# Kernel tuning notes

Hardware: AMD Instinct MI355X
Metric: run time of the kernel (lower is better)

## Reference

```python
import jax, jax.numpy as jnp
import numpy as np

NUM_NODES = 100000
NUM_HYPEREDGES = 20000
NUM_INCIDENCE = 1600000  # E: total (node, hyperedge) incidence entries
IN_CH = 128
OUT_CH = 128
EPS = 1e-6


def setup_inputs() -> dict:
    key = jax.random.key(0)
    k_x, k_row, k_col, k_w, k_b = jax.random.split(key, 5)
    x = jax.random.normal(k_x, (NUM_NODES, IN_CH), dtype=jnp.float32)
    node_idx = jax.random.randint(k_row, (NUM_INCIDENCE,), 0, NUM_NODES, dtype=jnp.int64)
    edge_idx = jax.random.randint(k_col, (NUM_INCIDENCE,), 0, NUM_HYPEREDGES, dtype=jnp.int64)
    hyperedge_index = jnp.stack([node_idx, edge_idx], axis=0)
    theta_w = jax.random.normal(k_w, (OUT_CH, IN_CH), dtype=jnp.float32) / np.sqrt(IN_CH)
    theta_b = jax.random.normal(k_b, (OUT_CH,), dtype=jnp.float32) * 0.01
    hyperedge_weight = jnp.ones((NUM_HYPEREDGES,), dtype=jnp.float32)
    return {"x": x, "hyperedge_index": hyperedge_index, "theta_w": theta_w,
            "theta_b": theta_b, "hyperedge_weight": hyperedge_weight}


def reference(x, hyperedge_index, theta_w, theta_b, hyperedge_weight):
    node_idx = hyperedge_index[0]  # [E]
    edge_idx = hyperedge_index[1]  # [E]
    ones_e = jnp.ones(node_idx.shape[0], dtype=x.dtype)

    # degree normalizers: B = hyperedge degrees, D = node degrees
    b_inv = 1.0 / (jax.ops.segment_sum(ones_e, edge_idx, num_segments=NUM_HYPEREDGES) + EPS)
    d_inv = 1.0 / (jax.ops.segment_sum(ones_e, node_idx, num_segments=NUM_NODES) + EPS)

    # X' = x @ Theta^T + b
    x_t = x @ theta_w.T + theta_b  # [N, out]

    # H^T X': scatter node features into hyperedges
    edge_feat = jax.ops.segment_sum(x_t[node_idx], edge_idx, num_segments=NUM_HYPEREDGES)
    edge_feat = edge_feat * (b_inv * hyperedge_weight)[:, None]  # [M, out]

    # H (W B^-1 H^T X'): scatter hyperedge features back to nodes
    node_agg = jax.ops.segment_sum(edge_feat[edge_idx], node_idx, num_segments=NUM_NODES)
    return node_agg * d_inv[:, None]  # [N, out]
```

## Files before the change

### kernel.cpp

```cpp
#include <hip/hip_runtime.h>

#define N_NODES 100000
#define N_EDGES 20000
#define CH 128
#define EPS 1e-6f

#define GEMM_BLOCKS ((N_NODES + 63) / 64)
#define NXCD 8
#define EPG ((N_EDGES + NXCD - 1) / NXCD)
#define NPG ((N_NODES + NXCD - 1) / NXCD)

#define CAP_E 192
#define CAP_N 64

typedef __attribute__((ext_vector_type(8))) short bf16x8;
typedef __attribute__((ext_vector_type(4))) float f32x4;

__device__ __forceinline__ unsigned short f2bf(float f) {
    unsigned int u = __float_as_uint(f);
    return (unsigned short)((u + 0x7FFFu + ((u >> 16) & 1u)) >> 16);
}
__device__ __forceinline__ float bflo(unsigned int u) { return __uint_as_float(u << 16); }
__device__ __forceinline__ float bfhi(unsigned int u) { return __uint_as_float(u & 0xFFFF0000u); }

__global__ __launch_bounds__(256) void wcvt_kernel(
    const float* __restrict__ w, unsigned short* __restrict__ wbf) {
    int i = blockIdx.x * 256 + threadIdx.x;
    if (i < CH * CH) wbf[i] = f2bf(w[i]);
}

__global__ __launch_bounds__(256) void gemm_kernel(
    const float* __restrict__ x, const unsigned short* __restrict__ wbf,
    const float* __restrict__ bias, unsigned short* __restrict__ xt) {

    const int l = threadIdx.x & 63;
    const int wv = threadIdx.x >> 6;
    const int rbase = blockIdx.x * 64 + wv * 16;
    const int arow = rbase + (l & 15);
    const int kb = (l >> 4) * 8;
    const bool rok = (arow < N_NODES);

    bf16x8 afr[4];
#pragma unroll
    for (int ks = 0; ks < 4; ++ks) {
        if (rok) {
            const float* xp = x + (size_t)arow * CH + ks * 32 + kb;
            float4 v0 = *(const float4*)xp;
            float4 v1 = *(const float4*)(xp + 4);
            afr[ks][0] = (short)f2bf(v0.x); afr[ks][1] = (short)f2bf(v0.y);
            afr[ks][2] = (short)f2bf(v0.z); afr[ks][3] = (short)f2bf(v0.w);
            afr[ks][4] = (short)f2bf(v1.x); afr[ks][5] = (short)f2bf(v1.y);
            afr[ks][6] = (short)f2bf(v1.z); afr[ks][7] = (short)f2bf(v1.w);
        } else {
#pragma unroll
            for (int i = 0; i < 8; ++i) afr[ks][i] = 0;
        }
    }

    const int r0 = (l >> 4) * 4;
#pragma unroll
    for (int nt = 0; nt < 8; ++nt) {
        const int bcol = nt * 16 + (l & 15);
        float bv = bias[bcol];
        f32x4 acc;
        acc[0] = bv; acc[1] = bv; acc[2] = bv; acc[3] = bv;
#pragma unroll
        for (int ks = 0; ks < 4; ++ks) {
            bf16x8 bfr = *(const bf16x8*)(wbf + (size_t)bcol * CH + ks * 32 + kb);
            acc = __builtin_amdgcn_mfma_f32_16x16x32_bf16(afr[ks], bfr, acc, 0, 0, 0);
        }
#pragma unroll
        for (int r = 0; r < 4; ++r) {
            int grow = rbase + r0 + r;
            if (grow < N_NODES)
                xt[(size_t)grow * CH + bcol] = f2bf(acc[r]);
        }
    }
}

__global__ __launch_bounds__(256) void fill_kernel(
    const int* __restrict__ node_idx, const int* __restrict__ edge_idx, int E,
    int* __restrict__ ecur, int* __restrict__ ncur,
    int* __restrict__ elist, int* __restrict__ nlist) {
    const int g = blockIdx.x & (NXCD - 1);
    const int wid = blockIdx.x >> 3;
    const int nblk = gridDim.x >> 3;
    const int elo = g * EPG, ehi = min(elo + EPG, N_EDGES);
    const int nlo = g * NPG, nhi = min(nlo + NPG, N_NODES);

    int i = wid * blockDim.x + threadIdx.x;
    const int stride = nblk * blockDim.x;
    for (; i < E; i += stride) {
        int e = edge_idx[i];
        int n = node_idx[i];
        if (e >= elo && e < ehi) {
            int p = atomicAdd(&ecur[e], 1);
            if (p < CAP_E) elist[(size_t)e * CAP_E + p] = n;
        }
        if (n >= nlo && n < nhi) {
            int q = atomicAdd(&ncur[n], 1);
            if (q < CAP_N) nlist[(size_t)n * CAP_N + q] = e;
        }
    }
}

__global__ __launch_bounds__(256) void edge_agg_kernel(
    const unsigned short* __restrict__ xt, const int* __restrict__ elist,
    const int* __restrict__ ecur, const float* __restrict__ hw,
    unsigned short* __restrict__ ef) {
    int wid = (blockIdx.x * blockDim.x + threadIdx.x) >> 6;
    int lane = threadIdx.x & 63;
    if (wid >= N_EDGES) return;
    int deg = ecur[wid];
    int len = min(deg, CAP_E);
    const int* seg = elist + (size_t)wid * CAP_E;
    float2 acc = make_float2(0.f, 0.f);
    for (int j0 = 0; j0 < len; j0 += 64) {
        int cnt = min(64, len - j0);
        int myn = (lane < cnt) ? seg[j0 + lane] : 0;
#pragma unroll 4
        for (int k = 0; k < cnt; ++k) {
            int n = __shfl(myn, k);
            unsigned int u = *(const unsigned int*)(xt + (size_t)n * CH + lane * 2);
            acc.x += bflo(u); acc.y += bfhi(u);
        }
    }
    float scale = hw[wid] / ((float)deg + EPS);
    unsigned int p = ((unsigned int)f2bf(acc.y * scale) << 16) | f2bf(acc.x * scale);
    *(unsigned int*)(ef + (size_t)wid * CH + lane * 2) = p;
}

__global__ __launch_bounds__(256) void node_agg_kernel(
    const unsigned short* __restrict__ ef, const int* __restrict__ nlist,
    const int* __restrict__ ncur, float* __restrict__ out) {
    int wid = (blockIdx.x * blockDim.x + threadIdx.x) >> 6;
    int lane = threadIdx.x & 63;
    if (wid >= N_NODES) return;
    int deg = ncur[wid];
    int len = min(deg, CAP_N);
    const int* seg = nlist + (size_t)wid * CAP_N;
    float2 acc = make_float2(0.f, 0.f);
    for (int j0 = 0; j0 < len; j0 += 64) {
        int cnt = min(64, len - j0);
        int mye = (lane < cnt) ? seg[j0 + lane] : 0;
#pragma unroll 4
        for (int k = 0; k < cnt; ++k) {
            int eg = __shfl(mye, k);
            unsigned int u = *(const unsigned int*)(ef + (size_t)eg * CH + lane * 2);
            acc.x += bflo(u); acc.y += bfhi(u);
        }
    }
    float dinv = 1.0f / ((float)deg + EPS);
    *(float2*)(out + (size_t)wid * CH + lane * 2) =
        make_float2(acc.x * dinv, acc.y * dinv);
}

extern "C" void kernel_launch(void* const* d_in, const int* in_sizes, int n_in,
                              void* d_out, int out_size, void* d_ws, size_t ws_size,
                              hipStream_t stream) {
    const float* x  = (const float*)d_in[0];
    const int*   hi = (const int*)d_in[1];
    const float* w  = (const float*)d_in[2];
    const float* b  = (const float*)d_in[3];
    const float* hw = (const float*)d_in[4];

    const int E = in_sizes[1] / 2;
    const int* node_idx = hi;
    const int* edge_idx = hi + E;

    unsigned short* xt  = (unsigned short*)d_ws;
    unsigned short* ef  = xt + (size_t)N_NODES * CH;
    unsigned short* wbf = ef + (size_t)N_EDGES * CH;
    int*   ecur   = (int*)(wbf + CH * CH);
    int*   ncur   = ecur + N_EDGES;
    int*   elist  = ncur + N_NODES;
    int*   nlist  = elist + (size_t)N_EDGES * CAP_E;

    hipMemsetAsync(ecur, 0, (size_t)(N_EDGES + N_NODES) * sizeof(int), stream);

    wcvt_kernel<<<(CH * CH + 255) / 256, 256, 0, stream>>>(w, wbf);

    gemm_kernel<<<GEMM_BLOCKS, 256, 0, stream>>>(x, wbf, b, xt);

    fill_kernel<<<2048, 256, 0, stream>>>(node_idx, edge_idx, E, ecur, ncur, elist, nlist);

    edge_agg_kernel<<<(N_EDGES * 64 + 255) / 256, 256, 0, stream>>>(
        xt, elist, ecur, hw, ef);
    node_agg_kernel<<<((size_t)N_NODES * 64 + 255) / 256, 256, 0, stream>>>(
        ef, nlist, ncur, (float*)d_out);
}
```

Measured before the change: 474.5 us.

## Split CSR fill into edge and node halves and overlap with GEMM and edge aggregation

```diff
diff --git a/kernel.cpp b/kernel.cpp
--- a/kernel.cpp
+++ b/kernel.cpp
@@ -9,6 +9,9 @@
 #define NXCD 8
 #define EPG ((N_EDGES + NXCD - 1) / NXCD)
 #define NPG ((N_NODES + NXCD - 1) / NXCD)
+#define FE_BLOCKS 1024
+#define FN_BLOCKS 1024
+#define EA_BLOCKS (N_EDGES * 64 / 256)
 
 #define CAP_E 192
 #define CAP_N 64
@@ -23,15 +26,29 @@
 __device__ __forceinline__ float bflo(unsigned int u) { return __uint_as_float(u << 16); }
 __device__ __forceinline__ float bfhi(unsigned int u) { return __uint_as_float(u & 0xFFFF0000u); }
 
-__global__ __launch_bounds__(256) void wcvt_kernel(
-    const float* __restrict__ w, unsigned short* __restrict__ wbf) {
-    int i = blockIdx.x * 256 + threadIdx.x;
-    if (i < CH * CH) wbf[i] = f2bf(w[i]);
-}
-
-__global__ __launch_bounds__(256) void gemm_kernel(
-    const float* __restrict__ x, const unsigned short* __restrict__ wbf,
-    const float* __restrict__ bias, unsigned short* __restrict__ xt) {
+__global__ __launch_bounds__(256) void gemm_fille_kernel(
+    const float* __restrict__ x, const float* __restrict__ w,
+    const float* __restrict__ bias, unsigned short* __restrict__ xt,
+    const int* __restrict__ node_idx, const int* __restrict__ edge_idx, int E,
+    int* __restrict__ ecur, int* __restrict__ elist) {
+
+    if (blockIdx.x >= GEMM_BLOCKS) {
+        const int b = blockIdx.x - GEMM_BLOCKS;
+        const int g = b & (NXCD - 1);
+        const int wid = b >> 3;
+        const int nblk = FE_BLOCKS >> 3;
+        const int elo = g * EPG, ehi = min(elo + EPG, N_EDGES);
+        int i = wid * 256 + threadIdx.x;
+        const int stride = nblk * 256;
+        for (; i < E; i += stride) {
+            int e = edge_idx[i];
+            if (e >= elo && e < ehi) {
+                int p = atomicAdd(&ecur[e], 1);
+                if (p < CAP_E) elist[(size_t)e * CAP_E + p] = node_idx[i];
+            }
+        }
+        return;
+    }
 
     const int l = threadIdx.x & 63;
     const int wv = threadIdx.x >> 6;
@@ -66,7 +83,14 @@
         acc[0] = bv; acc[1] = bv; acc[2] = bv; acc[3] = bv;
 #pragma unroll
         for (int ks = 0; ks < 4; ++ks) {
-            bf16x8 bfr = *(const bf16x8*)(wbf + (size_t)bcol * CH + ks * 32 + kb);
+            const float* wp = w + (size_t)bcol * CH + ks * 32 + kb;
+            float4 u0 = *(const float4*)wp;
+            float4 u1 = *(const float4*)(wp + 4);
+            bf16x8 bfr;
+            bfr[0] = (short)f2bf(u0.x); bfr[1] = (short)f2bf(u0.y);
+            bfr[2] = (short)f2bf(u0.z); bfr[3] = (short)f2bf(u0.w);
+            bfr[4] = (short)f2bf(u1.x); bfr[5] = (short)f2bf(u1.y);
+            bfr[6] = (short)f2bf(u1.z); bfr[7] = (short)f2bf(u1.w);
             acc = __builtin_amdgcn_mfma_f32_16x16x32_bf16(afr[ks], bfr, acc, 0, 0, 0);
         }
 #pragma unroll
@@ -78,37 +102,32 @@
     }
 }
 
-__global__ __launch_bounds__(256) void fill_kernel(
-    const int* __restrict__ node_idx, const int* __restrict__ edge_idx, int E,
-    int* __restrict__ ecur, int* __restrict__ ncur,
-    int* __restrict__ elist, int* __restrict__ nlist) {
-    const int g = blockIdx.x & (NXCD - 1);
-    const int wid = blockIdx.x >> 3;
-    const int nblk = gridDim.x >> 3;
-    const int elo = g * EPG, ehi = min(elo + EPG, N_EDGES);
-    const int nlo = g * NPG, nhi = min(nlo + NPG, N_NODES);
-
-    int i = wid * blockDim.x + threadIdx.x;
-    const int stride = nblk * blockDim.x;
-    for (; i < E; i += stride) {
-        int e = edge_idx[i];
-        int n = node_idx[i];
-        if (e >= elo && e < ehi) {
-            int p = atomicAdd(&ecur[e], 1);
-            if (p < CAP_E) elist[(size_t)e * CAP_E + p] = n;
-        }
-        if (n >= nlo && n < nhi) {
-            int q = atomicAdd(&ncur[n], 1);
-            if (q < CAP_N) nlist[(size_t)n * CAP_N + q] = e;
-        }
-    }
-}
-
-__global__ __launch_bounds__(256) void edge_agg_kernel(
+__global__ __launch_bounds__(256) void edgeagg_filln_kernel(
     const unsigned short* __restrict__ xt, const int* __restrict__ elist,
     const int* __restrict__ ecur, const float* __restrict__ hw,
-    unsigned short* __restrict__ ef) {
-    int wid = (blockIdx.x * blockDim.x + threadIdx.x) >> 6;
+    unsigned short* __restrict__ ef,
+    const int* __restrict__ node_idx, const int* __restrict__ edge_idx, int E,
+    int* __restrict__ ncur, int* __restrict__ nlist) {
+
+    if (blockIdx.x >= EA_BLOCKS) {
+        const int b = blockIdx.x - EA_BLOCKS;
+        const int g = b & (NXCD - 1);
+        const int wid = b >> 3;
+        const int nblk = FN_BLOCKS >> 3;
+        const int nlo = g * NPG, nhi = min(nlo + NPG, N_NODES);
+        int i = wid * 256 + threadIdx.x;
+        const int stride = nblk * 256;
+        for (; i < E; i += stride) {
+            int n = node_idx[i];
+            if (n >= nlo && n < nhi) {
+                int q = atomicAdd(&ncur[n], 1);
+                if (q < CAP_N) nlist[(size_t)n * CAP_N + q] = edge_idx[i];
+            }
+        }
+        return;
+    }
+
+    int wid = (blockIdx.x * 256 + threadIdx.x) >> 6;
     int lane = threadIdx.x & 63;
     if (wid >= N_EDGES) return;
     int deg = ecur[wid];
@@ -133,7 +152,7 @@
 __global__ __launch_bounds__(256) void node_agg_kernel(
     const unsigned short* __restrict__ ef, const int* __restrict__ nlist,
     const int* __restrict__ ncur, float* __restrict__ out) {
-    int wid = (blockIdx.x * blockDim.x + threadIdx.x) >> 6;
+    int wid = (blockIdx.x * 256 + threadIdx.x) >> 6;
     int lane = threadIdx.x & 63;
     if (wid >= N_NODES) return;
     int deg = ncur[wid];
@@ -170,22 +189,19 @@
 
     unsigned short* xt  = (unsigned short*)d_ws;
     unsigned short* ef  = xt + (size_t)N_NODES * CH;
-    unsigned short* wbf = ef + (size_t)N_EDGES * CH;
-    int*   ecur   = (int*)(wbf + CH * CH);
+    int*   ecur   = (int*)(ef + (size_t)N_EDGES * CH);
     int*   ncur   = ecur + N_EDGES;
     int*   elist  = ncur + N_NODES;
     int*   nlist  = elist + (size_t)N_EDGES * CAP_E;
 
     hipMemsetAsync(ecur, 0, (size_t)(N_EDGES + N_NODES) * sizeof(int), stream);
 
-    wcvt_kernel<<<(CH * CH + 255) / 256, 256, 0, stream>>>(w, wbf);
-
-    gemm_kernel<<<GEMM_BLOCKS, 256, 0, stream>>>(x, wbf, b, xt);
-
-    fill_kernel<<<2048, 256, 0, stream>>>(node_idx, edge_idx, E, ecur, ncur, elist, nlist);
-
-    edge_agg_kernel<<<(N_EDGES * 64 + 255) / 256, 256, 0, stream>>>(
-        xt, elist, ecur, hw, ef);
+    gemm_fille_kernel<<<GEMM_BLOCKS + FE_BLOCKS, 256, 0, stream>>>(
+        x, w, b, xt, node_idx, edge_idx, E, ecur, elist);
+
+    edgeagg_filln_kernel<<<EA_BLOCKS + FN_BLOCKS, 256, 0, stream>>>(
+        xt, elist, ecur, hw, ef, node_idx, edge_idx, E, ncur, nlist);
+
     node_agg_kernel<<<((size_t)N_NODES * 64 + 255) / 256, 256, 0, stream>>>(
         ef, nlist, ncur, (float*)d_out);
 }
```

Measured after the change: 470.0 us. No clear change (-1.0%).
